# Performance work log

Hardware: AMD Instinct MI355X
Metric: run time of the kernel (lower is better)

## Reference

```python
import jax, jax.numpy as jnp
import numpy as np

COUNTS = (16, 8, 8)  # num_scale_layers from __init__


def _conv1d(x, w, b):
    # x: [B, C, L], w: [Cout, Cin, K] (torch Conv1d layout), valid padding, stride 1
    y = jax.lax.conv_general_dilated(
        x, w, window_strides=(1,), padding='VALID',
        dimension_numbers=('NCH', 'OIH', 'NCH'))
    return y + b[None, :, None]


def _maxpool3s2(x):
    # MaxPool1d(kernel=3, stride=2), valid padding
    return jax.lax.reduce_window(x, -jnp.inf, jax.lax.max,
                                 (1, 1, 3), (1, 1, 2), 'VALID')


def setup_inputs() -> dict:
    key = jax.random.key(0)
    ks = jax.random.split(key, 5)
    B, C, N = 64, 512, 64
    scale = 0.03  # ~1/sqrt(C*K), keeps deep relu-conv chain numerically sane
    x = jax.random.normal(ks[0], (B, C, N), jnp.float32)
    w1 = jax.random.normal(ks[1], (C, C, 1), jnp.float32) * scale
    b1 = jax.random.normal(ks[2], (C,), jnp.float32) * scale
    n_k2 = sum(COUNTS) - len(COUNTS)  # 29 kernel-size-2 convs
    w2 = jax.random.normal(ks[3], (n_k2, C, C, 2), jnp.float32) * scale
    b2 = jax.random.normal(ks[4], (n_k2, C), jnp.float32) * scale
    return {"x": x, "w1": w1, "b1": b1, "w2": w2, "b2": b2}


def reference(x, w1, b1, w2, b2):
    B, C, N = x.shape
    x2d = jnp.zeros((B, C, N, N), x.dtype)
    mask = np.eye(N, dtype=bool)  # static: indices are compile-time constants
    k2 = 0
    stride, offset = 1, 0
    for level, count in enumerate(COUNTS):
        for order in range(count):
            if level == 0 and order == 0:
                x = jax.nn.relu(_conv1d(x, w1, b1))
            elif level > 0 and order == 0:
                x = jax.nn.relu(_maxpool3s2(x))
            else:
                x = jax.nn.relu(_conv1d(x, w2[k2], b2[k2]))
                k2 += 1
            i = np.arange(0, N - offset, stride)
            j = np.arange(offset, N, stride)
            # scatter conv output onto strided diagonal of the 2D map
            x2d = x2d.at[:, :, i, j].set(x)
            mask[i, j] = True
            offset += stride
        offset += stride
        stride *= 2
    return x2d, jnp.asarray(mask)
```

## Files before the change

kernel.cpp:

```cpp
#include <hip/hip_runtime.h>

typedef _Float16 f16;
typedef f16 f16x8 __attribute__((ext_vector_type(8)));
typedef f16 f16x4 __attribute__((ext_vector_type(4)));
typedef float f32x4 __attribute__((ext_vector_type(4)));

#define B_ 64
#define C_ 512
#define X2D_ELEMS ((size_t)134217728)
#define CHAIN_PITCH 1104

__device__ __forceinline__ int col_of(int i, int j) {
    const int d = j - i;
    if (d < 0) return -1;
    if (d <= 15) return 64 * d - (d * (d - 1)) / 2 + i;
    if (d >= 17 && d <= 31 && (d & 1) && !(i & 1)) {
        const int v = (d - 17) >> 1;
        return 904 + 24 * v - (v * (v - 1)) / 2 + (i >> 1);
    }
    if (d >= 35 && !((d - 35) & 3) && !(i & 3)) {
        const int v = (d - 35) >> 2;
        return 1068 + 8 * v - (v * (v - 1)) / 2 + (i >> 2);
    }
    return -1;
}

template<int K, int NF, int TAPS>
__device__ __forceinline__
void conv_split(const f16* S, const f16* __restrict__ wl,
                const float* __restrict__ bias, f16* __restrict__ chout,
                int Lin, int Lout, int m0)
{
    const int lane = threadIdx.x & 63, w = threadIdx.x >> 6;
    const int colq = lane & 15, kg = lane >> 4;
    const int mbase = m0 + w * 16;
    const f16* wp = wl + (size_t)(mbase + colq) * K + (kg << 3);

    int row[NF];
    #pragma unroll
    for (int nf = 0; nf < NF; nf++) {
        int c = nf * 16 + colq;
        if (c > Lin - TAPS) c = Lin - TAPS;
        row[nf] = c;
    }

    f32x4 acc[NF] = {};
    f16x8 a0 = *(const f16x8*)(wp);
    f16x8 a1 = *(const f16x8*)(wp + 32);
    f16x8 a2 = *(const f16x8*)(wp + 64);
    f16x8 a3 = *(const f16x8*)(wp + 96);

#define DO_STEP(AF, KK)                                                         \
    {                                                                           \
        const int t_ = (TAPS == 2 && (KK) >= 512) ? 1 : 0;                      \
        const int cch_ = (((KK) & 511) >> 3) + kg;                              \
        _Pragma("unroll")                                                       \
        for (int nf = 0; nf < NF; nf++) {                                       \
            const int r_ = row[nf] + t_;                                        \
            const f16x8 bf_ = *(const f16x8*)&S[(r_ << 9) + ((cch_ ^ (r_ & 7)) << 3)]; \
            acc[nf] = __builtin_amdgcn_mfma_f32_16x16x32_f16(AF, bf_, acc[nf], 0, 0, 0); \
        }                                                                       \
    }

    #pragma unroll
    for (int k0 = 0; k0 < K; k0 += 128) {
        DO_STEP(a0, k0);      if (k0 + 128 < K) a0 = *(const f16x8*)(wp + k0 + 128);
        DO_STEP(a1, k0 + 32); if (k0 + 128 < K) a1 = *(const f16x8*)(wp + k0 + 160);
        DO_STEP(a2, k0 + 64); if (k0 + 128 < K) a2 = *(const f16x8*)(wp + k0 + 192);
        DO_STEP(a3, k0 + 96); if (k0 + 128 < K) a3 = *(const f16x8*)(wp + k0 + 224);
    }
#undef DO_STEP

    const int co0 = mbase + (kg << 2);
    const float4 bb = *(const float4*)&bias[co0];
    #pragma unroll
    for (int nf = 0; nf < NF; nf++) {
        const int col = nf * 16 + colq;
        if (col < Lout) {
            f16x4 h;
            #pragma unroll
            for (int j = 0; j < 4; j++)
                h[j] = (f16)fmaxf(acc[nf][j] + ((const float*)&bb)[j], 0.0f);
            *(f16x4*)&chout[((size_t)col << 9) + co0] = h;
        }
    }
}

__global__ __launch_bounds__(256, 2)
void conv_l0_first(const float* __restrict__ x, const f16* __restrict__ Wf,
                   const float* __restrict__ b1, f16* __restrict__ chain)
{
    __shared__ __align__(16) f16 S[64 * 512];
    const int tid = threadIdx.x;
    const int b = blockIdx.x >> 3, q = blockIdx.x & 7;
    f16* chb = chain + (((size_t)b * CHAIN_PITCH) << 9);
    #pragma unroll 4
    for (int p = 0; p < 32; p++) {
        const int ci = p * 16 + (tid >> 4), l0 = (tid & 15) << 2;
        const float4 v = *(const float4*)&x[(((size_t)b * C_ + ci) << 6) + l0];
        #pragma unroll
        for (int j = 0; j < 4; j++) {
            const int r = l0 + j;
            S[(r << 9) + (((ci >> 3) ^ (r & 7)) << 3) + (ci & 7)] =
                (f16)((const float*)&v)[j];
        }
    }
    __syncthreads();
    conv_split<512, 4, 1>(S, Wf, b1, chb, 64, 64, q << 6);
}

__global__ __launch_bounds__(256, 2)
void conv_fused(const f16* __restrict__ xin, int cb_in,
                const f16* __restrict__ Wl, const float* __restrict__ bias,
                f16* __restrict__ chain, int cb_out,
                int Lin, int Lout, int G)
{
    constexpr int K = 1024;
    __shared__ f16 Bs[64 * 512];
    const int tid = threadIdx.x, lane = tid & 63, wv = tid >> 6;
    const int b0 = blockIdx.y * G, m0 = blockIdx.x * 64;
    const int rows = G * Lin;

    for (int r = wv; r < rows; r += 4) {
        const int g = r / Lin, l = r - g * Lin;
        const f16* src = xin + (((size_t)(b0 + g) * CHAIN_PITCH + cb_in + l) << 9);
        const f16x8 v = *(const f16x8*)(src + (lane << 3));
        *(f16x8*)&Bs[(r << 9) + ((lane ^ (r & 7)) << 3)] = v;
    }

    int vg[4], vl[4], row0[4]; bool val[4];
    #pragma unroll
    for (int nf = 0; nf < 4; nf++) {
        const int v = nf * 16 + (lane & 15);
        vg[nf] = v / Lout; vl[nf] = v - vg[nf] * Lout;
        val[nf] = vg[nf] < G;
        row0[nf] = val[nf] ? vg[nf] * Lin + vl[nf] : 0;
    }
    const int kg = lane >> 4;
    const f16* wp = Wl + (size_t)(m0 + wv * 16 + (lane & 15)) * K + (kg << 3);

    __syncthreads();

    f32x4 acc[4] = {};
    #pragma unroll 4
    for (int k0 = 0; k0 < K; k0 += 32) {
        const f16x8 af = *(const f16x8*)(wp + k0);
        const int t = (k0 >= 512) ? 1 : 0;
        const int cchunk = ((k0 & 511) >> 3) + kg;
        #pragma unroll
        for (int nf = 0; nf < 4; nf++) {
            const int r = row0[nf] + t;
            const f16x8 bf = *(const f16x8*)&Bs[(r << 9) + ((cchunk ^ (r & 7)) << 3)];
            acc[nf] = __builtin_amdgcn_mfma_f32_16x16x32_f16(af, bf, acc[nf], 0, 0, 0);
        }
    }

    const int co0 = m0 + wv * 16 + ((lane >> 4) << 2);
    const float4 bb = *(const float4*)&bias[co0];
    #pragma unroll
    for (int nf = 0; nf < 4; nf++) {
        if (!val[nf]) continue;
        f16x4 h;
        #pragma unroll
        for (int j = 0; j < 4; j++)
            h[j] = (f16)fmaxf(acc[nf][j] + ((const float*)&bb)[j], 0.0f);
        *(f16x4*)&chain[(((size_t)(b0 + vg[nf]) * CHAIN_PITCH + cb_out + vl[nf]) << 9) + co0] = h;
    }
}

__global__ void maxpool2(f16* __restrict__ chain, int cb_in, int cb_out)
{
    const int l = blockIdx.x, b = blockIdx.y, tid = threadIdx.x;
    const f16* s = chain + (((size_t)b * CHAIN_PITCH + cb_in + 2 * l) << 9) + 2 * tid;
    f16 o0 = (f16)fmaxf(fmaxf(fmaxf((float)s[0], (float)s[512]), (float)s[1024]), 0.0f);
    f16 o1 = (f16)fmaxf(fmaxf(fmaxf((float)s[1], (float)s[513]), (float)s[1025]), 0.0f);
    f16* d = &chain[(((size_t)b * CHAIN_PITCH + cb_out + l) << 9) + 2 * tid];
    d[0] = o0; d[1] = o1;
}

__global__ void prep_all(const float* __restrict__ w1, const float* __restrict__ w2,
                         f16* __restrict__ Wf, float* __restrict__ maskp)
{
    const unsigned idx = blockIdx.x * 256 + threadIdx.x;
    if (idx < 4096u)
        maskp[idx] = (col_of(idx >> 6, idx & 63) >= 0) ? 1.0f : 0.0f;
    if (idx < 262144u) {
        Wf[idx] = (f16)w1[idx];
    } else if (idx < 30u * 262144u) {
        const unsigned r = idx - 262144u;
        const int k2 = r >> 18;
        const unsigned rem = r & 262143u;
        const int co = rem >> 9, ci = rem & 511;
        const float2 v = *(const float2*)&w2[((((size_t)k2 << 9) + co) << 10) + (ci << 1)];
        f16* base = Wf + 262144 + ((size_t)k2 << 19) + ((size_t)co << 10);
        base[ci] = (f16)v.x;
        base[512 + ci] = (f16)v.y;
    }
}

__global__ __launch_bounds__(256)
void assemble3(const f16* __restrict__ chain, float* __restrict__ x2d)
{
    __shared__ __align__(16) f16 J[64 * 512];
    const int tid = threadIdx.x, lane = tid & 63, wv = tid >> 6;
    const int i = blockIdx.x, b = blockIdx.y;

    for (int j = wv; j < 64; j += 4) {
        const int col = col_of(i, j);
        f16x8 v = {0, 0, 0, 0, 0, 0, 0, 0};
        if (col >= 0)
            v = *(const f16x8*)(chain + (((size_t)b * CHAIN_PITCH + col) << 9) + (lane << 3));
        *(f16x8*)&J[(j << 9) + ((lane ^ (j & 7)) << 3)] = v;
    }
    __syncthreads();

    const int jq = tid & 15, c0 = tid >> 4;
    float* dst0 = x2d + (((size_t)b * C_) << 12) + (i << 6) + (jq << 2);
    for (int ct = 0; ct < 32; ct++) {
        const int c = c0 + (ct << 4);
        const int cj = c >> 3;
        float4 o;
        #pragma unroll
        for (int jj = 0; jj < 4; jj++) {
            const int j = (jq << 2) + jj;
            ((float*)&o)[jj] = (float)J[(j << 9) + ((cj ^ (j & 7)) << 3) + (c & 7)];
        }
        *(float4*)(dst0 + ((size_t)c << 12)) = o;
    }
}

extern "C" void kernel_launch(void* const* d_in, const int* in_sizes, int n_in,
                              void* d_out, int out_size, void* d_ws, size_t ws_size,
                              hipStream_t stream)
{
    const float* x  = (const float*)d_in[0];
    const float* w1 = (const float*)d_in[1];
    const float* b1 = (const float*)d_in[2];
    const float* w2 = (const float*)d_in[3];
    const float* b2 = (const float*)d_in[4];
    float* x2d   = (float*)d_out;
    float* maskp = x2d + X2D_ELEMS;

    f16* chain = (f16*)d_ws;
    f16* Wf    = (f16*)x2d;

    prep_all<<<(30 * 262144) / 256, 256, 0, stream>>>(w1, w2, Wf, maskp);

    conv_l0_first<<<512, 256, 0, stream>>>(x, Wf, b1, chain);

    const int counts[3] = {16, 8, 8};
    int L = 64, k2 = 0, cb = 64, prev = 0;
    for (int level = 0; level < 3; level++) {
        for (int order = 0; order < counts[level]; order++) {
            if (level == 0 && order == 0) continue;
            if (level > 0 && order == 0) {
                const int Lp = (L - 3) / 2 + 1;
                maxpool2<<<dim3(Lp, B_), 256, 0, stream>>>(chain, prev, cb);
                prev = cb; cb += Lp; L = Lp;
            } else {
                const int Lout = L - 1;
                int G = 1;
                while ((G * 2) * Lout <= 64 && (G * 2) * L <= 64) G *= 2;
                conv_fused<<<dim3(8, 64 / G), 256, 0, stream>>>(
                    chain, prev, Wf + 262144 + (size_t)k2 * 524288,
                    b2 + (size_t)k2 * C_, chain, cb, L, Lout, G);
                k2++; prev = cb; cb += Lout; L = Lout;
            }
        }
    }

    assemble3<<<dim3(64, B_), 256, 0, stream>>>(chain, x2d);
}
```

Baseline: 659.3 us.

## Fuse maxpool into following conv and widen per-wave output channel tile

Removes the standalone maxpool kernels by computing the pool while staging the next conv's input into shared memory, with one block column also writing the pooled result back to the chain. Each wave now computes 32 output channels instead of 16, sharing each shared-memory B fragment across two MFMA streams, and grids shrink to 4 channel blocks per batch group. The launch sequence is hard-coded per level. The result is fewer launches and fewer LDS reads per MFMA, at the cost of fewer blocks for occupancy and more accumulator registers.

```diff
diff --git a/kernel.cpp b/kernel.cpp
--- a/kernel.cpp
+++ b/kernel.cpp
@@ -25,75 +25,106 @@
     return -1;
 }
 
-template<int K, int NF, int TAPS>
+template<int K, int TAPS>
 __device__ __forceinline__
-void conv_split(const f16* S, const f16* __restrict__ wl,
-                const float* __restrict__ bias, f16* __restrict__ chout,
-                int Lin, int Lout, int m0)
+void conv_body(const f16* S, const f16* __restrict__ Wl,
+               const float* __restrict__ bias, f16* __restrict__ chain,
+               int b0, int q, int cb_out, int Lin, int Lout, int G)
 {
     const int lane = threadIdx.x & 63, w = threadIdx.x >> 6;
     const int colq = lane & 15, kg = lane >> 4;
-    const int mbase = m0 + w * 16;
-    const f16* wp = wl + (size_t)(mbase + colq) * K + (kg << 3);
-
-    int row[NF];
+    const int cobase = q * 128 + w * 32;
+    const f16* wp0 = Wl + (size_t)(cobase + colq) * K + (kg << 3);
+    const f16* wp1 = wp0 + (size_t)16 * K;
+
+    int vg[4], vl[4], row0[4]; bool val[4];
     #pragma unroll
-    for (int nf = 0; nf < NF; nf++) {
-        int c = nf * 16 + colq;
-        if (c > Lin - TAPS) c = Lin - TAPS;
-        row[nf] = c;
-    }
-
-    f32x4 acc[NF] = {};
-    f16x8 a0 = *(const f16x8*)(wp);
-    f16x8 a1 = *(const f16x8*)(wp + 32);
-    f16x8 a2 = *(const f16x8*)(wp + 64);
-    f16x8 a3 = *(const f16x8*)(wp + 96);
-
-#define DO_STEP(AF, KK)                                                         \
-    {                                                                           \
-        const int t_ = (TAPS == 2 && (KK) >= 512) ? 1 : 0;                      \
-        const int cch_ = (((KK) & 511) >> 3) + kg;                              \
-        _Pragma("unroll")                                                       \
-        for (int nf = 0; nf < NF; nf++) {                                       \
-            const int r_ = row[nf] + t_;                                        \
-            const f16x8 bf_ = *(const f16x8*)&S[(r_ << 9) + ((cch_ ^ (r_ & 7)) << 3)]; \
-            acc[nf] = __builtin_amdgcn_mfma_f32_16x16x32_f16(AF, bf_, acc[nf], 0, 0, 0); \
-        }                                                                       \
-    }
-
+    for (int nf = 0; nf < 4; nf++) {
+        const int v = nf * 16 + colq;
+        vg[nf] = v / Lout; vl[nf] = v - vg[nf] * Lout;
+        val[nf] = vg[nf] < G;
+        row0[nf] = val[nf] ? vg[nf] * Lin + vl[nf] : 0;
+    }
+
+    f32x4 acc0[4] = {}, acc1[4] = {};
+    #pragma unroll 4
+    for (int k0 = 0; k0 < K; k0 += 32) {
+        const f16x8 af0 = *(const f16x8*)(wp0 + k0);
+        const f16x8 af1 = *(const f16x8*)(wp1 + k0);
+        const int t = (TAPS == 2 && k0 >= 512) ? 1 : 0;
+        const int cch = ((k0 & 511) >> 3) + kg;
+        #pragma unroll
+        for (int nf = 0; nf < 4; nf++) {
+            const int r = row0[nf] + t;
+            const f16x8 bf = *(const f16x8*)&S[(r << 9) + ((cch ^ (r & 7)) << 3)];
+            acc0[nf] = __builtin_amdgcn_mfma_f32_16x16x32_f16(af0, bf, acc0[nf], 0, 0, 0);
+            acc1[nf] = __builtin_amdgcn_mfma_f32_16x16x32_f16(af1, bf, acc1[nf], 0, 0, 0);
+        }
+    }
+
+    const int co0 = cobase + (kg << 2);
+    const float4 bb0 = *(const float4*)&bias[co0];
+    const float4 bb1 = *(const float4*)&bias[co0 + 16];
     #pragma unroll
-    for (int k0 = 0; k0 < K; k0 += 128) {
-        DO_STEP(a0, k0);      if (k0 + 128 < K) a0 = *(const f16x8*)(wp + k0 + 128);
-        DO_STEP(a1, k0 + 32); if (k0 + 128 < K) a1 = *(const f16x8*)(wp + k0 + 160);
-        DO_STEP(a2, k0 + 64); if (k0 + 128 < K) a2 = *(const f16x8*)(wp + k0 + 192);
-        DO_STEP(a3, k0 + 96); if (k0 + 128 < K) a3 = *(const f16x8*)(wp + k0 + 224);
-    }
-#undef DO_STEP
-
-    const int co0 = mbase + (kg << 2);
-    const float4 bb = *(const float4*)&bias[co0];
-    #pragma unroll
-    for (int nf = 0; nf < NF; nf++) {
-        const int col = nf * 16 + colq;
-        if (col < Lout) {
-            f16x4 h;
+    for (int nf = 0; nf < 4; nf++) {
+        if (!val[nf]) continue;
+        const size_t base = (((size_t)(b0 + vg[nf]) * CHAIN_PITCH + cb_out + vl[nf]) << 9);
+        f16x4 h0, h1;
+        #pragma unroll
+        for (int j = 0; j < 4; j++) {
+            h0[j] = (f16)fmaxf(acc0[nf][j] + ((const float*)&bb0)[j], 0.0f);
+            h1[j] = (f16)fmaxf(acc1[nf][j] + ((const float*)&bb1)[j], 0.0f);
+        }
+        *(f16x4*)&chain[base + co0] = h0;
+        *(f16x4*)&chain[base + co0 + 16] = h1;
+    }
+}
+
+template<int POOL>
+__global__ __launch_bounds__(256, 2)
+void conv_k2(const f16* __restrict__ chainr, int cb_in,
+             const f16* __restrict__ Wl, const float* __restrict__ bias,
+             f16* __restrict__ chain, int cb_pool, int cb_out,
+             int Lin, int Lout, int G)
+{
+    __shared__ __align__(16) f16 S[64 * 512];
+    const int lane = threadIdx.x & 63, wv = threadIdx.x >> 6;
+    const int b0 = blockIdx.x * G, q = blockIdx.y;
+    const int rows = G * Lin;
+
+    for (int r = wv; r < rows; r += 4) {
+        const int g = r / Lin, l = r - g * Lin;
+        f16x8 o;
+        if (POOL) {
+            const f16* src = chainr +
+                (((size_t)(b0 + g) * CHAIN_PITCH + cb_in + 2 * l) << 9) + (lane << 3);
+            const f16x8 s0 = *(const f16x8*)(src);
+            const f16x8 s1 = *(const f16x8*)(src + 512);
+            const f16x8 s2 = *(const f16x8*)(src + 1024);
             #pragma unroll
-            for (int j = 0; j < 4; j++)
-                h[j] = (f16)fmaxf(acc[nf][j] + ((const float*)&bb)[j], 0.0f);
-            *(f16x4*)&chout[((size_t)col << 9) + co0] = h;
-        }
-    }
+            for (int j = 0; j < 8; j++)
+                o[j] = (f16)fmaxf(fmaxf((float)s0[j], (float)s1[j]),
+                                  fmaxf((float)s2[j], 0.0f));
+            if (q == 0)
+                *(f16x8*)&chain[(((size_t)(b0 + g) * CHAIN_PITCH + cb_pool + l) << 9)
+                                + (lane << 3)] = o;
+        } else {
+            o = *(const f16x8*)(chainr +
+                (((size_t)(b0 + g) * CHAIN_PITCH + cb_in + l) << 9) + (lane << 3));
+        }
+        *(f16x8*)&S[(r << 9) + ((lane ^ (r & 7)) << 3)] = o;
+    }
+    __syncthreads();
+    conv_body<1024, 2>(S, Wl, bias, chain, b0, q, cb_out, Lin, Lout, G);
 }
 
 __global__ __launch_bounds__(256, 2)
-void conv_l0_first(const float* __restrict__ x, const f16* __restrict__ Wf,
-                   const float* __restrict__ b1, f16* __restrict__ chain)
+void conv_first(const float* __restrict__ x, const f16* __restrict__ Wf,
+                const float* __restrict__ b1, f16* __restrict__ chain)
 {
     __shared__ __align__(16) f16 S[64 * 512];
     const int tid = threadIdx.x;
-    const int b = blockIdx.x >> 3, q = blockIdx.x & 7;
-    f16* chb = chain + (((size_t)b * CHAIN_PITCH) << 9);
+    const int b = blockIdx.x, q = blockIdx.y;
     #pragma unroll 4
     for (int p = 0; p < 32; p++) {
         const int ci = p * 16 + (tid >> 4), l0 = (tid & 15) << 2;
@@ -106,76 +137,7 @@
         }
     }
     __syncthreads();
-    conv_split<512, 4, 1>(S, Wf, b1, chb, 64, 64, q << 6);
-}
-
-__global__ __launch_bounds__(256, 2)
-void conv_fused(const f16* __restrict__ xin, int cb_in,
-                const f16* __restrict__ Wl, const float* __restrict__ bias,
-                f16* __restrict__ chain, int cb_out,
-                int Lin, int Lout, int G)
-{
-    constexpr int K = 1024;
-    __shared__ f16 Bs[64 * 512];
-    const int tid = threadIdx.x, lane = tid & 63, wv = tid >> 6;
-    const int b0 = blockIdx.y * G, m0 = blockIdx.x * 64;
-    const int rows = G * Lin;
-
-    for (int r = wv; r < rows; r += 4) {
-        const int g = r / Lin, l = r - g * Lin;
-        const f16* src = xin + (((size_t)(b0 + g) * CHAIN_PITCH + cb_in + l) << 9);
-        const f16x8 v = *(const f16x8*)(src + (lane << 3));
-        *(f16x8*)&Bs[(r << 9) + ((lane ^ (r & 7)) << 3)] = v;
-    }
-
-    int vg[4], vl[4], row0[4]; bool val[4];
-    #pragma unroll
-    for (int nf = 0; nf < 4; nf++) {
-        const int v = nf * 16 + (lane & 15);
-        vg[nf] = v / Lout; vl[nf] = v - vg[nf] * Lout;
-        val[nf] = vg[nf] < G;
-        row0[nf] = val[nf] ? vg[nf] * Lin + vl[nf] : 0;
-    }
-    const int kg = lane >> 4;
-    const f16* wp = Wl + (size_t)(m0 + wv * 16 + (lane & 15)) * K + (kg << 3);
-
-    __syncthreads();
-
-    f32x4 acc[4] = {};
-    #pragma unroll 4
-    for (int k0 = 0; k0 < K; k0 += 32) {
-        const f16x8 af = *(const f16x8*)(wp + k0);
-        const int t = (k0 >= 512) ? 1 : 0;
-        const int cchunk = ((k0 & 511) >> 3) + kg;
-        #pragma unroll
-        for (int nf = 0; nf < 4; nf++) {
-            const int r = row0[nf] + t;
-            const f16x8 bf = *(const f16x8*)&Bs[(r << 9) + ((cchunk ^ (r & 7)) << 3)];
-            acc[nf] = __builtin_amdgcn_mfma_f32_16x16x32_f16(af, bf, acc[nf], 0, 0, 0);
-        }
-    }
-
-    const int co0 = m0 + wv * 16 + ((lane >> 4) << 2);
-    const float4 bb = *(const float4*)&bias[co0];
-    #pragma unroll
-    for (int nf = 0; nf < 4; nf++) {
-        if (!val[nf]) continue;
-        f16x4 h;
-        #pragma unroll
-        for (int j = 0; j < 4; j++)
-            h[j] = (f16)fmaxf(acc[nf][j] + ((const float*)&bb)[j], 0.0f);
-        *(f16x4*)&chain[(((size_t)(b0 + vg[nf]) * CHAIN_PITCH + cb_out + vl[nf]) << 9) + co0] = h;
-    }
-}
-
-__global__ void maxpool2(f16* __restrict__ chain, int cb_in, int cb_out)
-{
-    const int l = blockIdx.x, b = blockIdx.y, tid = threadIdx.x;
-    const f16* s = chain + (((size_t)b * CHAIN_PITCH + cb_in + 2 * l) << 9) + 2 * tid;
-    f16 o0 = (f16)fmaxf(fmaxf(fmaxf((float)s[0], (float)s[512]), (float)s[1024]), 0.0f);
-    f16 o1 = (f16)fmaxf(fmaxf(fmaxf((float)s[1], (float)s[513]), (float)s[1025]), 0.0f);
-    f16* d = &chain[(((size_t)b * CHAIN_PITCH + cb_out + l) << 9) + 2 * tid];
-    d[0] = o0; d[1] = o1;
+    conv_body<512, 1>(S, Wf, b1, chain, b, q, 0, 64, 64, 1);
 }
 
 __global__ void prep_all(const float* __restrict__ w1, const float* __restrict__ w2,
@@ -246,27 +208,36 @@
 
     prep_all<<<(30 * 262144) / 256, 256, 0, stream>>>(w1, w2, Wf, maskp);
 
-    conv_l0_first<<<512, 256, 0, stream>>>(x, Wf, b1, chain);
-
-    const int counts[3] = {16, 8, 8};
-    int L = 64, k2 = 0, cb = 64, prev = 0;
-    for (int level = 0; level < 3; level++) {
-        for (int order = 0; order < counts[level]; order++) {
-            if (level == 0 && order == 0) continue;
-            if (level > 0 && order == 0) {
-                const int Lp = (L - 3) / 2 + 1;
-                maxpool2<<<dim3(Lp, B_), 256, 0, stream>>>(chain, prev, cb);
-                prev = cb; cb += Lp; L = Lp;
-            } else {
-                const int Lout = L - 1;
-                int G = 1;
-                while ((G * 2) * Lout <= 64 && (G * 2) * L <= 64) G *= 2;
-                conv_fused<<<dim3(8, 64 / G), 256, 0, stream>>>(
-                    chain, prev, Wf + 262144 + (size_t)k2 * 524288,
-                    b2 + (size_t)k2 * C_, chain, cb, L, Lout, G);
-                k2++; prev = cb; cb += Lout; L = Lout;
-            }
-        }
+    conv_first<<<dim3(64, 4), 256, 0, stream>>>(x, Wf, b1, chain);
+
+    int L = 64, cb = 64, prev = 0, k2 = 0;
+    for (int i = 0; i < 15; i++) {
+        conv_k2<0><<<dim3(64, 4), 256, 0, stream>>>(
+            chain, prev, Wf + 262144 + (size_t)k2 * 524288, b2 + (size_t)k2 * C_,
+            chain, 0, cb, L, L - 1, 1);
+        k2++; prev = cb; cb += L - 1; L--;
+    }
+
+    conv_k2<1><<<dim3(32, 4), 256, 0, stream>>>(
+        chain, prev, Wf + 262144 + (size_t)k2 * 524288, b2 + (size_t)k2 * C_,
+        chain, 904, 928, 24, 23, 2);
+    k2++; L = 23; prev = 928; cb = 951;
+    for (int i = 0; i < 6; i++) {
+        conv_k2<0><<<dim3(32, 4), 256, 0, stream>>>(
+            chain, prev, Wf + 262144 + (size_t)k2 * 524288, b2 + (size_t)k2 * C_,
+            chain, 0, cb, L, L - 1, 2);
+        k2++; prev = cb; cb += L - 1; L--;
+    }
+
+    conv_k2<1><<<dim3(8, 4), 256, 0, stream>>>(
+        chain, prev, Wf + 262144 + (size_t)k2 * 524288, b2 + (size_t)k2 * C_,
+        chain, 1068, 1076, 8, 7, 8);
+    k2++; L = 7; prev = 1076; cb = 1083;
+    for (int i = 0; i < 6; i++) {
+        conv_k2<0><<<dim3(8, 4), 256, 0, stream>>>(
+            chain, prev, Wf + 262144 + (size_t)k2 * 524288, b2 + (size_t)k2 * C_,
+            chain, 0, cb, L, L - 1, 8);
+        k2++; prev = cb; cb += L - 1; L--;
     }
 
     assemble3<<<dim3(64, B_), 256, 0, stream>>>(chain, x2d);
```

After: 759.4 us. +15.2%, slower.
